# Performance work log

Hardware: AMD Instinct MI355X
Metric: run time of the kernel (lower is better)

The kernel has to match this reference:

```python
import jax, jax.numpy as jnp
import numpy as np

N_NODES = 100000
N_EDGES = 300000
N_GRAPHS = 2048
F_ATOM = 40
D_IN = 128    # GINInputSize
D_HID = 256   # GINHiddenSize
D_OUT = 512   # FPSize
D_TASK = 1    # OutputSize


def _glorot(key, shape):
    fan_in, fan_out = shape[0], shape[1]
    lim = (6.0 / (fan_in + fan_out)) ** 0.5
    return jax.random.uniform(key, shape, jnp.float32, -lim, lim)


def setup_inputs() -> dict:
    key = jax.random.key(0)
    ks = jax.random.split(key, 16)
    inp = {
        'x': jax.random.normal(ks[0], (N_NODES, F_ATOM), jnp.float32),
        'edge_index': jax.random.randint(ks[1], (2, N_EDGES), 0, N_NODES, jnp.int64),
        'batch': jnp.sort(jax.random.randint(ks[2], (N_NODES,), 0, N_GRAPHS, jnp.int64)),
        # NodeFeatEmbed: MLP([F_ATOM, D_IN]) == single Linear (plain_last)
        'W_embed': _glorot(ks[3], (F_ATOM, D_IN)),
        'b_embed': jnp.zeros((D_IN,), jnp.float32),
        # GINConv eps per layer (train_eps=False -> 0.0 constants)
        'eps': jnp.zeros((3,), jnp.float32),
        # layer 0: MLP([D_IN, D_HID, D_HID])
        'W1_0': _glorot(ks[4], (D_IN, D_HID)),  'b1_0': jnp.zeros((D_HID,), jnp.float32),
        'W2_0': _glorot(ks[5], (D_HID, D_HID)), 'b2_0': jnp.zeros((D_HID,), jnp.float32),
        # layer 1: MLP([D_HID, D_HID, D_HID])
        'W1_1': _glorot(ks[6], (D_HID, D_HID)), 'b1_1': jnp.zeros((D_HID,), jnp.float32),
        'W2_1': _glorot(ks[7], (D_HID, D_HID)), 'b2_1': jnp.zeros((D_HID,), jnp.float32),
        # layer 2 (last, maps to out_channels=FPSize): MLP([D_HID, D_OUT, D_OUT])
        'W1_2': _glorot(ks[8], (D_HID, D_OUT)), 'b1_2': jnp.zeros((D_OUT,), jnp.float32),
        'W2_2': _glorot(ks[9], (D_OUT, D_OUT)), 'b2_2': jnp.zeros((D_OUT,), jnp.float32),
        # task head
        'W_task': _glorot(ks[10], (D_OUT, D_TASK)),
        'b_task': jnp.zeros((D_TASK,), jnp.float32),
    }
    return inp


def _gin_forward(x, edge_index, batch, W_embed, b_embed, eps, layers, W_task, b_task):
    src, dst = edge_index[0], edge_index[1]
    # NodeFeatEmbed
    h = x @ W_embed + b_embed                                    # [N, D_IN]
    n_layers = len(layers)
    for l, (W1, b1, W2, b2) in enumerate(layers):
        # GINConv: MLP((1+eps)*h + sum_{j->i} h_j)
        agg = jax.ops.segment_sum(h[src], dst, num_segments=N_NODES)
        z = (1.0 + eps[l]) * h + agg
        h = jax.nn.relu(z @ W1 + b1) @ W2 + b2
        if l < n_layers - 1:                                     # inter-layer act (not after last)
            h = jax.nn.relu(h)
    # global_add_pool readout
    pooled = jax.ops.segment_sum(h, batch, num_segments=N_GRAPHS)  # [G, D_OUT]
    return pooled @ W_task + b_task                               # [G, D_TASK]


def reference(x, edge_index, batch, W_embed, b_embed, eps,
              W1_0, b1_0, W2_0, b2_0,
              W1_1, b1_1, W2_1, b2_1,
              W1_2, b1_2, W2_2, b2_2,
              W_task, b_task):
    layers = [(W1_0, b1_0, W2_0, b2_0), (W1_1, b1_1, W2_1, b2_1), (W1_2, b1_2, W2_2, b2_2)]
    return _gin_forward(x, edge_index, batch, W_embed, b_embed, eps, layers, W_task, b_task)
```

## Files before the change

kernel.cpp:

```cpp
#include <hip/hip_runtime.h>

#define N_NODES 100000
#define E_EDGES 300000
#define N_GRAPHS 2048

typedef float  floatx4 __attribute__((ext_vector_type(4)));
typedef short  shortx8 __attribute__((ext_vector_type(8)));

__device__ __forceinline__ float bf2f(unsigned short u) {
  return __uint_as_float(((unsigned int)u) << 16);
}
__device__ __forceinline__ unsigned short f2bf(float f) {
  unsigned int u = __float_as_uint(f);
  u += 0x7FFFu + ((u >> 16) & 1u);
  return (unsigned short)(u >> 16);
}

__device__ __forceinline__ void cp16(const void* g, void* l) {
  __builtin_amdgcn_global_load_lds(
      (const __attribute__((address_space(1))) unsigned int*)g,
      (__attribute__((address_space(3))) unsigned int*)l, 16, 0, 0);
}

struct PrepArgs {
  const float* W[4];
  unsigned short* Wt[4];
  int K[4];
  int N[4];
  const float* We;
  const float* be;
  const float* W1_0;
  unsigned short* WfT;
  const float* W2_2;
  const float* b2_2;
  const float* wtask;
  float* w2v;
  float* c2;
  float* nodedot;
  float* out;
  const float* b_task;
};

__global__ __launch_bounds__(256)
void prep_kernel(PrepArgs a) {
  const int blk = blockIdx.x;
  if (blk < 320) {
    int z, b;
    if (blk < 64)       { z = 0; b = blk; }
    else if (blk < 128) { z = 1; b = blk - 64; }
    else if (blk < 192) { z = 2; b = blk - 128; }
    else                { z = 3; b = blk - 192; }
    const int K = a.K[z], N = a.N[z];
    const int nt = N / 32;
    const int kb = (b / nt) * 32, nb = (b % nt) * 32;
    __shared__ unsigned short tile[32][33];
    const float* W = a.W[z];
    unsigned short* Wt = a.Wt[z];
    const int tx = threadIdx.x & 31, ty = threadIdx.x >> 5;
    for (int r = ty; r < 32; r += 8)
      tile[r][tx] = f2bf(W[(size_t)(kb + r) * N + nb + tx]);
    __syncthreads();
    for (int r = ty; r < 32; r += 8)
      Wt[(size_t)(nb + r) * K + kb + tx] = tile[tx][r];
  } else if (blk < 361) {
    const int k = blk - 320;
    const int n = threadIdx.x;
    if (k < 40) {
      float s = 0.f;
      for (int j = 0; j < 128; j++) s = fmaf(a.We[k * 128 + j], a.W1_0[(size_t)j * 256 + n], s);
      a.WfT[n * 64 + k] = f2bf(s);
    } else {
      float s = 0.f;
      for (int j = 0; j < 128; j++) s = fmaf(a.be[j], a.W1_0[(size_t)j * 256 + n], s);
      a.WfT[n * 64 + 40] = f2bf(s);
      for (int kk = 41; kk < 64; kk++) a.WfT[n * 64 + kk] = 0;
    }
  } else if (blk < 490) {
    const int p = blk - 361;
    const int lane = threadIdx.x & 63;
    const int wave = threadIdx.x >> 6;
    if (p < 128) {
      const int k = p * 4 + wave;
      const float* row = a.W2_2 + (size_t)k * 512 + lane * 8;
      float4 a0 = *(const float4*)(row);
      float4 a1 = *(const float4*)(row + 4);
      float4 w0 = *(const float4*)(a.wtask + lane * 8);
      float4 w1 = *(const float4*)(a.wtask + lane * 8 + 4);
      float s = a0.x * w0.x + a0.y * w0.y + a0.z * w0.z + a0.w * w0.w +
                a1.x * w1.x + a1.y * w1.y + a1.z * w1.z + a1.w * w1.w;
#pragma unroll
      for (int off = 32; off > 0; off >>= 1) s += __shfl_down(s, off);
      if (lane == 0) a.w2v[k] = s;
    } else if (wave == 0) {
      float4 a0 = *(const float4*)(a.b2_2 + lane * 8);
      float4 a1 = *(const float4*)(a.b2_2 + lane * 8 + 4);
      float4 w0 = *(const float4*)(a.wtask + lane * 8);
      float4 w1 = *(const float4*)(a.wtask + lane * 8 + 4);
      float s = a0.x * w0.x + a0.y * w0.y + a0.z * w0.z + a0.w * w0.w +
                a1.x * w1.x + a1.y * w1.y + a1.z * w1.z + a1.w * w1.w;
#pragma unroll
      for (int off = 32; off > 0; off >>= 1) s += __shfl_down(s, off);
      if (lane == 0) *a.c2 = s;
    }
  } else if (blk < 881) {
    int i = (blk - 490) * 256 + threadIdx.x;
    if (i < N_NODES) a.nodedot[i] = 0.f;
  } else {
    int g = (blk - 881) * 256 + threadIdx.x;
    if (g < N_GRAPHS) a.out[g] = a.b_task[0];
  }
}

__global__ __launch_bounds__(256)
void zero_kernel(int* __restrict__ p, int n) {
  int i = blockIdx.x * 256 + threadIdx.x;
  if (i < n) p[i] = 0;
}

__global__ __launch_bounds__(256)
void hist_kernel(const int* __restrict__ ei, int* __restrict__ deg) {
  int e = blockIdx.x * 256 + threadIdx.x;
  if (e < E_EDGES) atomicAdd(&deg[ei[E_EDGES + e]], 1);
}

__global__ __launch_bounds__(256)
void scan_blk_kernel(const int* __restrict__ in, int* __restrict__ out,
                     int* __restrict__ blk_sums, int n_in, int n_out) {
  __shared__ int sm[256];
  const int t = threadIdx.x;
  const int base = blockIdx.x * 1024 + t * 4;
  int d0 = (base + 0 < n_in) ? in[base + 0] : 0;
  int d1 = (base + 1 < n_in) ? in[base + 1] : 0;
  int d2 = (base + 2 < n_in) ? in[base + 2] : 0;
  int d3 = (base + 3 < n_in) ? in[base + 3] : 0;
  int s = d0 + d1 + d2 + d3;
  sm[t] = s;
  __syncthreads();
  for (int off = 1; off < 256; off <<= 1) {
    int v = (t >= off) ? sm[t - off] : 0;
    __syncthreads();
    sm[t] += v;
    __syncthreads();
  }
  int excl = sm[t] - s;
  if (base + 0 < n_out) out[base + 0] = excl;
  if (base + 1 < n_out) out[base + 1] = excl + d0;
  if (base + 2 < n_out) out[base + 2] = excl + d0 + d1;
  if (base + 3 < n_out) out[base + 3] = excl + d0 + d1 + d2;
  if (t == 255 && blk_sums) blk_sums[blockIdx.x] = sm[255];
}

__global__ __launch_bounds__(256)
void scan_fix_kernel(int* __restrict__ row_ptr, const int* __restrict__ blk_off,
                     int* __restrict__ cursor) {
  int i = blockIdx.x * 256 + threadIdx.x;
  if (i <= N_NODES) {
    int v = row_ptr[i] + blk_off[i >> 10];
    row_ptr[i] = v;
    if (i < N_NODES) cursor[i] = v;
  }
}

__global__ __launch_bounds__(256)
void fill_kernel(const int* __restrict__ ei, int* __restrict__ cursor,
                 int* __restrict__ csr_src) {
  int e = blockIdx.x * 256 + threadIdx.x;
  if (e < E_EDGES) {
    int d = ei[E_EDGES + e];
    int slot = atomicAdd(&cursor[d], 1);
    csr_src[slot] = ei[e];
  }
}

__global__ __launch_bounds__(256)
void gatherx_kernel(const float* __restrict__ X, unsigned short* __restrict__ G,
                    const int* __restrict__ row_ptr, const int* __restrict__ csr,
                    const float* __restrict__ eps) {
  const int node = blockIdx.x * 4 + (threadIdx.x >> 6);
  const int lane = threadIdx.x & 63;
  const float sc = 1.0f + eps[0];
  const int e0 = row_ptr[node];
  const int e1 = row_ptr[node + 1];
  float acc = 0.f;
  if (lane < 40) {
    acc = sc * X[(size_t)node * 40 + lane];
    int e = e0;
    for (; e + 4 <= e1; e += 4) {
      int s0 = csr[e], s1 = csr[e + 1], s2 = csr[e + 2], s3 = csr[e + 3];
      float a0 = X[(size_t)s0 * 40 + lane];
      float a1 = X[(size_t)s1 * 40 + lane];
      float a2 = X[(size_t)s2 * 40 + lane];
      float a3 = X[(size_t)s3 * 40 + lane];
      acc += (a0 + a1) + (a2 + a3);
    }
    for (; e < e1; e++)
      acc += X[(size_t)csr[e] * 40 + lane];
  } else if (lane == 40) {
    acc = sc + (float)(e1 - e0);
  }
  G[(size_t)node * 64 + lane] = f2bf(acc);
}

__global__ __launch_bounds__(256)
void gather_kernel(const unsigned short* __restrict__ H, unsigned short* __restrict__ Z,
                   const int* __restrict__ row_ptr, const int* __restrict__ csr,
                   const float* __restrict__ eps, int l) {
  const int node = blockIdx.x * 4 + (threadIdx.x >> 6);
  const int lane = threadIdx.x & 63;
  const float sc = 1.0f + eps[l];
  uint2 hv = *(const uint2*)(H + (size_t)node * 256 + lane * 4);
  float acc[4];
  acc[0] = sc * bf2f((unsigned short)(hv.x & 0xFFFF));
  acc[1] = sc * bf2f((unsigned short)(hv.x >> 16));
  acc[2] = sc * bf2f((unsigned short)(hv.y & 0xFFFF));
  acc[3] = sc * bf2f((unsigned short)(hv.y >> 16));
  const int e0 = row_ptr[node];
  const int e1 = row_ptr[node + 1];
  int e = e0;
  for (; e + 2 <= e1; e += 2) {
    int s0 = csr[e], s1 = csr[e + 1];
    uint2 a = *(const uint2*)(H + (size_t)s0 * 256 + lane * 4);
    uint2 b = *(const uint2*)(H + (size_t)s1 * 256 + lane * 4);
    acc[0] += bf2f((unsigned short)(a.x & 0xFFFF)) + bf2f((unsigned short)(b.x & 0xFFFF));
    acc[1] += bf2f((unsigned short)(a.x >> 16))    + bf2f((unsigned short)(b.x >> 16));
    acc[2] += bf2f((unsigned short)(a.y & 0xFFFF)) + bf2f((unsigned short)(b.y & 0xFFFF));
    acc[3] += bf2f((unsigned short)(a.y >> 16))    + bf2f((unsigned short)(b.y >> 16));
  }
  if (e < e1) {
    int s0 = csr[e];
    uint2 a = *(const uint2*)(H + (size_t)s0 * 256 + lane * 4);
    acc[0] += bf2f((unsigned short)(a.x & 0xFFFF));
    acc[1] += bf2f((unsigned short)(a.x >> 16));
    acc[2] += bf2f((unsigned short)(a.y & 0xFFFF));
    acc[3] += bf2f((unsigned short)(a.y >> 16));
  }
  unsigned short z[4] = {f2bf(acc[0]), f2bf(acc[1]), f2bf(acc[2]), f2bf(acc[3])};
  *(uint2*)(Z + (size_t)node * 256 + lane * 4) = *(uint2*)z;
}

template <int K1>
__global__ __launch_bounds__(256, 3)
void fused_mlp_kernel(const unsigned short* __restrict__ A,
                      const unsigned short* __restrict__ W1t,
                      const float* __restrict__ b1,
                      const unsigned short* __restrict__ W2t,
                      const float* __restrict__ b2,
                      unsigned short* __restrict__ H,
                      int M) {
  constexpr int ACH = K1 / 8;
  constexpr int ZP = (64 * ACH) / 256;

  __shared__ uint4 smem4[3072];
  unsigned short* Bs = (unsigned short*)smem4;
  unsigned short* Ts = (unsigned short*)(smem4 + 1024);

  const int m0 = blockIdx.x * 64;
  const int tid = threadIdx.x;
  const int lane = tid & 63;
  const int wave = tid >> 6;
  const int fr = lane & 15;
  const int fq = lane >> 4;
  const int wn = wave * 64;

#pragma unroll
  for (int p = 0; p < ZP; p++) {
    int slot = p * 256 + tid;
    int row = slot / ACH;
    int cs = slot % ACH;
    int cg = cs ^ (row & 7);
    int grow = m0 + row;
    if (grow >= M) grow = M - 1;
    cp16(A + (size_t)grow * K1 + cg * 8, Ts + (size_t)(p * 256 + wn) * 8);
  }

  const int bn_ = tid >> 2;
  const int bc_ = tid & 3;
  const unsigned short* srcW1[4];
  const unsigned short* srcW2[4];
#pragma unroll
  for (int p = 0; p < 4; p++) {
    int n = p * 64 + bn_;
    int sw = (bc_ ^ ((n >> 1) & 3)) << 3;
    srcW1[p] = W1t + (size_t)n * K1 + sw;
    srcW2[p] = W2t + (size_t)n * 256 + sw;
  }

  int offB[4];
#pragma unroll
  for (int j = 0; j < 4; j++) {
    int n = wn + j * 16 + fr;
    offB[j] = n * 32 + ((fq ^ ((n >> 1) & 3)) << 3);
  }

  floatx4 acc[4][4];
#pragma unroll
  for (int i = 0; i < 4; i++)
#pragma unroll
    for (int j = 0; j < 4; j++) acc[i][j] = (floatx4){0.f, 0.f, 0.f, 0.f};

  for (int k0 = 0; k0 < K1; k0 += 32) {
#pragma unroll
    for (int p = 0; p < 4; p++)
      cp16(srcW1[p] + k0, Bs + (size_t)(p * 256 + wn) * 8);
    __syncthreads();
    shortx8 af[4], bv[4];
    const int kc = k0 >> 3;
#pragma unroll
    for (int i = 0; i < 4; i++) {
      int row = i * 16 + fr;
      af[i] = *(const shortx8*)&Ts[row * K1 + (((kc + fq) ^ (fr & 7)) << 3)];
    }
#pragma unroll
    for (int j = 0; j < 4; j++) bv[j] = *(const shortx8*)&Bs[offB[j]];
#pragma unroll
    for (int i = 0; i < 4; i++)
#pragma unroll
      for (int j = 0; j < 4; j++)
        acc[i][j] = __builtin_amdgcn_mfma_f32_16x16x32_bf16(af[i], bv[j], acc[i][j], 0, 0, 0);
    __syncthreads();
  }

#pragma unroll
  for (int j = 0; j < 4; j++) {
    int col = wn + j * 16 + fr;
    float bb = b1[col];
    int cgc = col >> 3, c7 = col & 7;
#pragma unroll
    for (int i = 0; i < 4; i++)
#pragma unroll
      for (int r = 0; r < 4; r++) {
        int row = i * 16 + fq * 4 + r;
        float v = fmaxf(acc[i][j][r] + bb, 0.f);
        Ts[row * 256 + (((cgc ^ (row & 7)) << 3) | c7)] = f2bf(v);
        acc[i][j][r] = 0.f;
      }
  }

  for (int k0 = 0; k0 < 256; k0 += 32) {
#pragma unroll
    for (int p = 0; p < 4; p++)
      cp16(srcW2[p] + k0, Bs + (size_t)(p * 256 + wn) * 8);
    __syncthreads();
    shortx8 af[4], bv[4];
    const int kc = k0 >> 3;
#pragma unroll
    for (int i = 0; i < 4; i++) {
      int row = i * 16 + fr;
      af[i] = *(const shortx8*)&Ts[row * 256 + (((kc + fq) ^ (fr & 7)) << 3)];
    }
#pragma unroll
    for (int j = 0; j < 4; j++) bv[j] = *(const shortx8*)&Bs[offB[j]];
#pragma unroll
    for (int i = 0; i < 4; i++)
#pragma unroll
      for (int j = 0; j < 4; j++)
        acc[i][j] = __builtin_amdgcn_mfma_f32_16x16x32_bf16(af[i], bv[j], acc[i][j], 0, 0, 0);
    __syncthreads();
  }

#pragma unroll
  for (int j = 0; j < 4; j++) {
    int col = wn + j * 16 + fr;
    float bb = b2[col];
    int cgc = col >> 3, c7 = col & 7;
#pragma unroll
    for (int i = 0; i < 4; i++)
#pragma unroll
      for (int r = 0; r < 4; r++) {
        int row = i * 16 + fq * 4 + r;
        float v = fmaxf(acc[i][j][r] + bb, 0.f);
        Ts[row * 256 + (((cgc ^ (row & 7)) << 3) | c7)] = f2bf(v);
      }
  }
  __syncthreads();
  const int r2 = tid >> 5;
  const int cg2 = tid & 31;
#pragma unroll
  for (int p = 0; p < 8; p++) {
    int row = p * 8 + r2;
    int grow = m0 + row;
    if (grow < M) {
      uint4 v = *(const uint4*)&Ts[row * 256 + ((cg2 ^ (row & 7)) << 3)];
      *(uint4*)&H[(size_t)grow * 256 + cg2 * 8] = v;
    }
  }
}

__global__ __launch_bounds__(256, 3)
void fused_dot_kernel(const unsigned short* __restrict__ A,
                      const unsigned short* __restrict__ W1t,
                      const float* __restrict__ b1,
                      const float* __restrict__ w2v,
                      float* __restrict__ nodedot, int M) {
  __shared__ uint4 smem4[3072];
  unsigned short* Bs = (unsigned short*)smem4;
  unsigned short* Ts = (unsigned short*)(smem4 + 1024);

  const int m0 = blockIdx.x * 64;
  const int tid = threadIdx.x;
  const int lane = tid & 63;
  const int wave = tid >> 6;
  const int fr = lane & 15;
  const int fq = lane >> 4;
  const int wn = wave * 64;

#pragma unroll
  for (int p = 0; p < 8; p++) {
    int slot = p * 256 + tid;
    int row = slot >> 5;
    int cs = slot & 31;
    int cg = cs ^ (row & 7);
    int grow = m0 + row;
    if (grow >= M) grow = M - 1;
    cp16(A + (size_t)grow * 256 + cg * 8, Ts + (size_t)(p * 256 + wn) * 8);
  }

  const int bn_ = tid >> 2;
  const int bc_ = tid & 3;
  const unsigned short* srcW[4];
#pragma unroll
  for (int p = 0; p < 4; p++) {
    int n = p * 64 + bn_;
    srcW[p] = W1t + (size_t)n * 256 + ((bc_ ^ ((n >> 1) & 3)) << 3);
  }
  int offB[4];
#pragma unroll
  for (int j = 0; j < 4; j++) {
    int n = wn + j * 16 + fr;
    offB[j] = n * 32 + ((fq ^ ((n >> 1) & 3)) << 3);
  }

  float pd[4][4];
#pragma unroll
  for (int i = 0; i < 4; i++)
#pragma unroll
    for (int r = 0; r < 4; r++) pd[i][r] = 0.f;

  for (int nh = 0; nh < 2; nh++) {
    floatx4 acc[4][4];
#pragma unroll
    for (int i = 0; i < 4; i++)
#pragma unroll
      for (int j = 0; j < 4; j++) acc[i][j] = (floatx4){0.f, 0.f, 0.f, 0.f};
    const size_t nhoff = (size_t)nh * 256 * 256;
    for (int k0 = 0; k0 < 256; k0 += 32) {
#pragma unroll
      for (int p = 0; p < 4; p++)
        cp16(srcW[p] + nhoff + k0, Bs + (size_t)(p * 256 + wn) * 8);
      __syncthreads();
      shortx8 af[4], bv[4];
      const int kc = k0 >> 3;
#pragma unroll
      for (int i = 0; i < 4; i++) {
        int row = i * 16 + fr;
        af[i] = *(const shortx8*)&Ts[row * 256 + (((kc + fq) ^ (fr & 7)) << 3)];
      }
#pragma unroll
      for (int j = 0; j < 4; j++) bv[j] = *(const shortx8*)&Bs[offB[j]];
#pragma unroll
      for (int i = 0; i < 4; i++)
#pragma unroll
        for (int j = 0; j < 4; j++)
          acc[i][j] = __builtin_amdgcn_mfma_f32_16x16x32_bf16(af[i], bv[j], acc[i][j], 0, 0, 0);
      __syncthreads();
    }
#pragma unroll
    for (int j = 0; j < 4; j++) {
      int col = nh * 256 + wn + j * 16 + fr;
      float bb = b1[col];
      float wv = w2v[col];
#pragma unroll
      for (int i = 0; i < 4; i++)
#pragma unroll
        for (int r = 0; r < 4; r++)
          pd[i][r] += fmaxf(acc[i][j][r] + bb, 0.f) * wv;
    }
  }

#pragma unroll
  for (int i = 0; i < 4; i++)
#pragma unroll
    for (int r = 0; r < 4; r++) {
      float s = pd[i][r];
#pragma unroll
      for (int off = 1; off < 16; off <<= 1) s += __shfl_xor(s, off);
      if (fr == 0) {
        int row = m0 + i * 16 + fq * 4 + r;
        if (row < M) unsafeAtomicAdd(&nodedot[row], s);
      }
    }
}

__global__ __launch_bounds__(256)
void pool_kernel(const float* __restrict__ nodedot, const int* __restrict__ batch,
                 float* __restrict__ out, const float* __restrict__ c2p) {
  int t = blockIdx.x * 256 + threadIdx.x;
  int i0 = t * 64;
  if (i0 >= N_NODES) return;
  int i1 = i0 + 64;
  if (i1 > N_NODES) i1 = N_NODES;
  const float c2 = *c2p;
  int g = batch[i0];
  float s = 0.f;
  for (int i = i0; i < i1; i++) {
    int gi = batch[i];
    if (gi != g) { unsafeAtomicAdd(&out[g], s); g = gi; s = 0.f; }
    s += nodedot[i] + c2;
  }
  unsafeAtomicAdd(&out[g], s);
}

extern "C" void kernel_launch(void* const* d_in, const int* in_sizes, int n_in,
                              void* d_out, int out_size, void* d_ws, size_t ws_size,
                              hipStream_t stream) {
  const float* x       = (const float*)d_in[0];
  const int*   ei      = (const int*)d_in[1];
  const int*   batch   = (const int*)d_in[2];
  const float* W_embed = (const float*)d_in[3];
  const float* b_embed = (const float*)d_in[4];
  const float* eps     = (const float*)d_in[5];
  const float* W1[3] = {(const float*)d_in[6],  (const float*)d_in[10], (const float*)d_in[14]};
  const float* B1[3] = {(const float*)d_in[7],  (const float*)d_in[11], (const float*)d_in[15]};
  const float* W2[3] = {(const float*)d_in[8],  (const float*)d_in[12], (const float*)d_in[16]};
  const float* B2[3] = {(const float*)d_in[9],  (const float*)d_in[13], (const float*)d_in[17]};
  const float* W_task = (const float*)d_in[18];
  const float* b_task = (const float*)d_in[19];
  float* out = (float*)d_out;

  const size_t OFF_RZ  = 102400000;
  const size_t OFF_AUX = 153600000;
  if (ws_size < OFF_AUX + 4000000) return;
  unsigned short* RH = (unsigned short*)d_ws;
  unsigned short* RZ = (unsigned short*)((char*)d_ws + OFF_RZ);
  char* aux = (char*)d_ws + OFF_AUX;
  int* row_ptr  = (int*)(aux);
  int* cursor   = (int*)(aux + 400016);
  int* csr_src  = (int*)(aux + 800016);
  int* blk_sums = (int*)(aux + 2000016);
  int* blk_off  = (int*)(aux + 2000416);
  float* nodedot = (float*)(aux + 2000816);
  unsigned short* WT = (unsigned short*)(aux + 2400832);
  float* w2v = (float*)(aux + 3200832);
  float* c2  = (float*)(aux + 3202880);
  unsigned short* WfT    = WT;
  unsigned short* Wt2_0  = WT + 32768;
  unsigned short* Wt1_1  = WT + 98304;
  unsigned short* Wt2_1  = WT + 163840;
  unsigned short* Wt1_2  = WT + 229376;

  PrepArgs pa;
  pa.W[0] = W2[0]; pa.Wt[0] = Wt2_0; pa.K[0] = 256; pa.N[0] = 256;
  pa.W[1] = W1[1]; pa.Wt[1] = Wt1_1; pa.K[1] = 256; pa.N[1] = 256;
  pa.W[2] = W2[1]; pa.Wt[2] = Wt2_1; pa.K[2] = 256; pa.N[2] = 256;
  pa.W[3] = W1[2]; pa.Wt[3] = Wt1_2; pa.K[3] = 256; pa.N[3] = 512;
  pa.We = W_embed; pa.be = b_embed; pa.W1_0 = W1[0]; pa.WfT = WfT;
  pa.W2_2 = W2[2]; pa.b2_2 = B2[2]; pa.wtask = W_task; pa.w2v = w2v; pa.c2 = c2;
  pa.nodedot = nodedot; pa.out = out; pa.b_task = b_task;
  prep_kernel<<<889, 256, 0, stream>>>(pa);

  zero_kernel<<<(N_NODES + 255) / 256, 256, 0, stream>>>(cursor, N_NODES);
  hist_kernel<<<(E_EDGES + 255) / 256, 256, 0, stream>>>(ei, cursor);
  scan_blk_kernel<<<98, 256, 0, stream>>>(cursor, row_ptr, blk_sums, N_NODES, N_NODES + 1);
  scan_blk_kernel<<<1, 256, 0, stream>>>(blk_sums, blk_off, nullptr, 98, 98);
  scan_fix_kernel<<<(N_NODES + 256) / 256, 256, 0, stream>>>(row_ptr, blk_off, cursor);
  fill_kernel<<<(E_EDGES + 255) / 256, 256, 0, stream>>>(ei, cursor, csr_src);

  const int FB = (N_NODES + 63) / 64;

  gatherx_kernel<<<N_NODES / 4, 256, 0, stream>>>(x, RZ, row_ptr, csr_src, eps);
  fused_mlp_kernel<64><<<FB, 256, 0, stream>>>(RZ, WfT, B1[0], Wt2_0, B2[0], RH, N_NODES);

  gather_kernel<<<N_NODES / 4, 256, 0, stream>>>(RH, RZ, row_ptr, csr_src, eps, 1);
  fused_mlp_kernel<256><<<FB, 256, 0, stream>>>(RZ, Wt1_1, B1[1], Wt2_1, B2[1], RH, N_NODES);

  gather_kernel<<<N_NODES / 4, 256, 0, stream>>>(RH, RZ, row_ptr, csr_src, eps, 2);
  fused_dot_kernel<<<FB, 256, 0, stream>>>(RZ, Wt1_2, B1[2], w2v, nodedot, N_NODES);

  pool_kernel<<<((N_NODES + 63) / 64 + 255) / 256, 256, 0, stream>>>(nodedot, batch, out, c2);
}
```

Baseline: 422.0 us.

## Load weight fragments directly from global memory instead of staging through LDS

Both fused MLP kernels now read the B-operand (weight) fragments for the MFMA straight from global memory into registers, instead of copying each 32-wide K slice into a shared buffer. This drops the per-iteration barriers, shrinks LDS use from 48 KB to 32 KB, and fully unrolls the K loops. The aim is to remove the synchronisation and LDS traffic in the inner loop and allow more blocks per CU. The cost is that each wave issues its own global loads for weights, relying on L1/L2 hits, and load latency is exposed inside the unrolled loop.

```diff
diff --git a/kernel.cpp b/kernel.cpp
--- a/kernel.cpp
+++ b/kernel.cpp
@@ -250,9 +250,7 @@
   constexpr int ACH = K1 / 8;
   constexpr int ZP = (64 * ACH) / 256;
 
-  __shared__ uint4 smem4[3072];
-  unsigned short* Bs = (unsigned short*)smem4;
-  unsigned short* Ts = (unsigned short*)(smem4 + 1024);
+  __shared__ unsigned short Ts[64 * 256];
 
   const int m0 = blockIdx.x * 64;
   const int tid = threadIdx.x;
@@ -273,23 +271,13 @@
     cp16(A + (size_t)grow * K1 + cg * 8, Ts + (size_t)(p * 256 + wn) * 8);
   }
 
-  const int bn_ = tid >> 2;
-  const int bc_ = tid & 3;
-  const unsigned short* srcW1[4];
-  const unsigned short* srcW2[4];
-#pragma unroll
-  for (int p = 0; p < 4; p++) {
-    int n = p * 64 + bn_;
-    int sw = (bc_ ^ ((n >> 1) & 3)) << 3;
-    srcW1[p] = W1t + (size_t)n * K1 + sw;
-    srcW2[p] = W2t + (size_t)n * 256 + sw;
-  }
-
-  int offB[4];
+  const unsigned short* wb1[4];
+  const unsigned short* wb2[4];
 #pragma unroll
   for (int j = 0; j < 4; j++) {
     int n = wn + j * 16 + fr;
-    offB[j] = n * 32 + ((fq ^ ((n >> 1) & 3)) << 3);
+    wb1[j] = W1t + (size_t)n * K1 + fq * 8;
+    wb2[j] = W2t + (size_t)n * 256 + fq * 8;
   }
 
   floatx4 acc[4][4];
@@ -298,27 +286,26 @@
 #pragma unroll
     for (int j = 0; j < 4; j++) acc[i][j] = (floatx4){0.f, 0.f, 0.f, 0.f};
 
+  __syncthreads();
+
+#pragma unroll
   for (int k0 = 0; k0 < K1; k0 += 32) {
-#pragma unroll
-    for (int p = 0; p < 4; p++)
-      cp16(srcW1[p] + k0, Bs + (size_t)(p * 256 + wn) * 8);
-    __syncthreads();
     shortx8 af[4], bv[4];
     const int kc = k0 >> 3;
+#pragma unroll
+    for (int j = 0; j < 4; j++) bv[j] = *(const shortx8*)(wb1[j] + k0);
 #pragma unroll
     for (int i = 0; i < 4; i++) {
       int row = i * 16 + fr;
       af[i] = *(const shortx8*)&Ts[row * K1 + (((kc + fq) ^ (fr & 7)) << 3)];
     }
 #pragma unroll
-    for (int j = 0; j < 4; j++) bv[j] = *(const shortx8*)&Bs[offB[j]];
-#pragma unroll
     for (int i = 0; i < 4; i++)
 #pragma unroll
       for (int j = 0; j < 4; j++)
         acc[i][j] = __builtin_amdgcn_mfma_f32_16x16x32_bf16(af[i], bv[j], acc[i][j], 0, 0, 0);
-    __syncthreads();
-  }
+  }
+  __syncthreads();
 
 #pragma unroll
   for (int j = 0; j < 4; j++) {
@@ -335,28 +322,26 @@
         acc[i][j][r] = 0.f;
       }
   }
-
+  __syncthreads();
+
+#pragma unroll
   for (int k0 = 0; k0 < 256; k0 += 32) {
-#pragma unroll
-    for (int p = 0; p < 4; p++)
-      cp16(srcW2[p] + k0, Bs + (size_t)(p * 256 + wn) * 8);
-    __syncthreads();
     shortx8 af[4], bv[4];
     const int kc = k0 >> 3;
+#pragma unroll
+    for (int j = 0; j < 4; j++) bv[j] = *(const shortx8*)(wb2[j] + k0);
 #pragma unroll
     for (int i = 0; i < 4; i++) {
       int row = i * 16 + fr;
       af[i] = *(const shortx8*)&Ts[row * 256 + (((kc + fq) ^ (fr & 7)) << 3)];
     }
 #pragma unroll
-    for (int j = 0; j < 4; j++) bv[j] = *(const shortx8*)&Bs[offB[j]];
-#pragma unroll
     for (int i = 0; i < 4; i++)
 #pragma unroll
       for (int j = 0; j < 4; j++)
         acc[i][j] = __builtin_amdgcn_mfma_f32_16x16x32_bf16(af[i], bv[j], acc[i][j], 0, 0, 0);
-    __syncthreads();
-  }
+  }
+  __syncthreads();
 
 #pragma unroll
   for (int j = 0; j < 4; j++) {
@@ -392,9 +377,7 @@
                       const float* __restrict__ b1,
                       const float* __restrict__ w2v,
                       float* __restrict__ nodedot, int M) {
-  __shared__ uint4 smem4[3072];
-  unsigned short* Bs = (unsigned short*)smem4;
-  unsigned short* Ts = (unsigned short*)(smem4 + 1024);
+  __shared__ unsigned short Ts[64 * 256];
 
   const int m0 = blockIdx.x * 64;
   const int tid = threadIdx.x;
@@ -415,54 +398,42 @@
     cp16(A + (size_t)grow * 256 + cg * 8, Ts + (size_t)(p * 256 + wn) * 8);
   }
 
-  const int bn_ = tid >> 2;
-  const int bc_ = tid & 3;
-  const unsigned short* srcW[4];
-#pragma unroll
-  for (int p = 0; p < 4; p++) {
-    int n = p * 64 + bn_;
-    srcW[p] = W1t + (size_t)n * 256 + ((bc_ ^ ((n >> 1) & 3)) << 3);
-  }
-  int offB[4];
-#pragma unroll
-  for (int j = 0; j < 4; j++) {
-    int n = wn + j * 16 + fr;
-    offB[j] = n * 32 + ((fq ^ ((n >> 1) & 3)) << 3);
-  }
-
   float pd[4][4];
 #pragma unroll
   for (int i = 0; i < 4; i++)
 #pragma unroll
     for (int r = 0; r < 4; r++) pd[i][r] = 0.f;
 
+  __syncthreads();
+
   for (int nh = 0; nh < 2; nh++) {
+    const unsigned short* wb[4];
+#pragma unroll
+    for (int j = 0; j < 4; j++) {
+      int n = nh * 256 + wn + j * 16 + fr;
+      wb[j] = W1t + (size_t)n * 256 + fq * 8;
+    }
     floatx4 acc[4][4];
 #pragma unroll
     for (int i = 0; i < 4; i++)
 #pragma unroll
       for (int j = 0; j < 4; j++) acc[i][j] = (floatx4){0.f, 0.f, 0.f, 0.f};
-    const size_t nhoff = (size_t)nh * 256 * 256;
+#pragma unroll
     for (int k0 = 0; k0 < 256; k0 += 32) {
-#pragma unroll
-      for (int p = 0; p < 4; p++)
-        cp16(srcW[p] + nhoff + k0, Bs + (size_t)(p * 256 + wn) * 8);
-      __syncthreads();
       shortx8 af[4], bv[4];
       const int kc = k0 >> 3;
+#pragma unroll
+      for (int j = 0; j < 4; j++) bv[j] = *(const shortx8*)(wb[j] + k0);
 #pragma unroll
       for (int i = 0; i < 4; i++) {
         int row = i * 16 + fr;
         af[i] = *(const shortx8*)&Ts[row * 256 + (((kc + fq) ^ (fr & 7)) << 3)];
       }
 #pragma unroll
-      for (int j = 0; j < 4; j++) bv[j] = *(const shortx8*)&Bs[offB[j]];
-#pragma unroll
       for (int i = 0; i < 4; i++)
 #pragma unroll
         for (int j = 0; j < 4; j++)
           acc[i][j] = __builtin_amdgcn_mfma_f32_16x16x32_bf16(af[i], bv[j], acc[i][j], 0, 0, 0);
-      __syncthreads();
     }
 #pragma unroll
     for (int j = 0; j < 4; j++) {
```

Result: slower. 520.5 us (+23.3%).

## Double-buffer weight tiles in fused MLP kernels and drop node-dot atomics

Applied to the files above, without the earlier changes.

Weight k-tiles in LDS are now double-buffered in the fused MLP and fused dot kernels, so the next tile's async global-to-LDS copy overlaps the current MFMA step. The W2 prefetch is chained onto the end of the W1 loop. Each wave of the dot kernel writes its partial node dot to a separate slab instead of atomically adding into one array, and the pool kernel sums the four slabs. The larger LDS footprint forces launch bounds down to 2 blocks per CU, trading occupancy for overlap.

```diff
diff --git a/kernel.cpp b/kernel.cpp
--- a/kernel.cpp
+++ b/kernel.cpp
@@ -239,7 +239,7 @@
 }
 
 template <int K1>
-__global__ __launch_bounds__(256, 3)
+__global__ __launch_bounds__(256, 2)
 void fused_mlp_kernel(const unsigned short* __restrict__ A,
                       const unsigned short* __restrict__ W1t,
                       const float* __restrict__ b1,
@@ -249,10 +249,10 @@
                       int M) {
   constexpr int ACH = K1 / 8;
   constexpr int ZP = (64 * ACH) / 256;
-
-  __shared__ uint4 smem4[3072];
-  unsigned short* Bs = (unsigned short*)smem4;
-  unsigned short* Ts = (unsigned short*)(smem4 + 1024);
+  constexpr int NT1 = K1 / 32;
+
+  __shared__ unsigned short Bs[2][256 * 32];
+  __shared__ unsigned short Ts[64 * 256];
 
   const int m0 = blockIdx.x * 64;
   const int tid = threadIdx.x;
@@ -292,32 +292,45 @@
     offB[j] = n * 32 + ((fq ^ ((n >> 1) & 3)) << 3);
   }
 
+#pragma unroll
+  for (int p = 0; p < 4; p++)
+    cp16(srcW1[p], &Bs[0][(size_t)(p * 256 + wn) * 8]);
+
   floatx4 acc[4][4];
 #pragma unroll
   for (int i = 0; i < 4; i++)
 #pragma unroll
     for (int j = 0; j < 4; j++) acc[i][j] = (floatx4){0.f, 0.f, 0.f, 0.f};
 
-  for (int k0 = 0; k0 < K1; k0 += 32) {
-#pragma unroll
-    for (int p = 0; p < 4; p++)
-      cp16(srcW1[p] + k0, Bs + (size_t)(p * 256 + wn) * 8);
-    __syncthreads();
+  __syncthreads();
+  int buf = 0;
+
+  for (int t = 0; t < NT1; t++) {
+    if (t + 1 < NT1) {
+#pragma unroll
+      for (int p = 0; p < 4; p++)
+        cp16(srcW1[p] + (t + 1) * 32, &Bs[buf ^ 1][(size_t)(p * 256 + wn) * 8]);
+    } else {
+#pragma unroll
+      for (int p = 0; p < 4; p++)
+        cp16(srcW2[p], &Bs[buf ^ 1][(size_t)(p * 256 + wn) * 8]);
+    }
     shortx8 af[4], bv[4];
-    const int kc = k0 >> 3;
+    const int kc = t * 4;
 #pragma unroll
     for (int i = 0; i < 4; i++) {
       int row = i * 16 + fr;
       af[i] = *(const shortx8*)&Ts[row * K1 + (((kc + fq) ^ (fr & 7)) << 3)];
     }
 #pragma unroll
-    for (int j = 0; j < 4; j++) bv[j] = *(const shortx8*)&Bs[offB[j]];
+    for (int j = 0; j < 4; j++) bv[j] = *(const shortx8*)&Bs[buf][offB[j]];
 #pragma unroll
     for (int i = 0; i < 4; i++)
 #pragma unroll
       for (int j = 0; j < 4; j++)
         acc[i][j] = __builtin_amdgcn_mfma_f32_16x16x32_bf16(af[i], bv[j], acc[i][j], 0, 0, 0);
     __syncthreads();
+    buf ^= 1;
   }
 
 #pragma unroll
@@ -335,27 +348,30 @@
         acc[i][j][r] = 0.f;
       }
   }
-
-  for (int k0 = 0; k0 < 256; k0 += 32) {
-#pragma unroll
-    for (int p = 0; p < 4; p++)
-      cp16(srcW2[p] + k0, Bs + (size_t)(p * 256 + wn) * 8);
-    __syncthreads();
+  __syncthreads();
+
+  for (int t = 0; t < 8; t++) {
+    if (t + 1 < 8) {
+#pragma unroll
+      for (int p = 0; p < 4; p++)
+        cp16(srcW2[p] + (t + 1) * 32, &Bs[buf ^ 1][(size_t)(p * 256 + wn) * 8]);
+    }
     shortx8 af[4], bv[4];
-    const int kc = k0 >> 3;
+    const int kc = t * 4;
 #pragma unroll
     for (int i = 0; i < 4; i++) {
       int row = i * 16 + fr;
       af[i] = *(const shortx8*)&Ts[row * 256 + (((kc + fq) ^ (fr & 7)) << 3)];
     }
 #pragma unroll
-    for (int j = 0; j < 4; j++) bv[j] = *(const shortx8*)&Bs[offB[j]];
+    for (int j = 0; j < 4; j++) bv[j] = *(const shortx8*)&Bs[buf][offB[j]];
 #pragma unroll
     for (int i = 0; i < 4; i++)
 #pragma unroll
       for (int j = 0; j < 4; j++)
         acc[i][j] = __builtin_amdgcn_mfma_f32_16x16x32_bf16(af[i], bv[j], acc[i][j], 0, 0, 0);
     __syncthreads();
+    buf ^= 1;
   }
 
 #pragma unroll
@@ -386,15 +402,14 @@
   }
 }
 
-__global__ __launch_bounds__(256, 3)
+__global__ __launch_bounds__(256, 2)
 void fused_dot_kernel(const unsigned short* __restrict__ A,
                       const unsigned short* __restrict__ W1t,
                       const float* __restrict__ b1,
                       const float* __restrict__ w2v,
-                      float* __restrict__ nodedot, int M) {
-  __shared__ uint4 smem4[3072];
-  unsigned short* Bs = (unsigned short*)smem4;
-  unsigned short* Ts = (unsigned short*)(smem4 + 1024);
+                      float* __restrict__ nodedot4, int M) {
+  __shared__ unsigned short Bs[2][256 * 32];
+  __shared__ unsigned short Ts[64 * 256];
 
   const int m0 = blockIdx.x * 64;
   const int tid = threadIdx.x;
@@ -430,50 +445,65 @@
     offB[j] = n * 32 + ((fq ^ ((n >> 1) & 3)) << 3);
   }
 
+#pragma unroll
+  for (int p = 0; p < 4; p++)
+    cp16(srcW[p], &Bs[0][(size_t)(p * 256 + wn) * 8]);
+
   float pd[4][4];
 #pragma unroll
   for (int i = 0; i < 4; i++)
 #pragma unroll
     for (int r = 0; r < 4; r++) pd[i][r] = 0.f;
 
-  for (int nh = 0; nh < 2; nh++) {
-    floatx4 acc[4][4];
+  floatx4 acc[4][4];
+#pragma unroll
+  for (int i = 0; i < 4; i++)
+#pragma unroll
+    for (int j = 0; j < 4; j++) acc[i][j] = (floatx4){0.f, 0.f, 0.f, 0.f};
+
+  __syncthreads();
+  int buf = 0;
+
+  for (int s = 0; s < 16; s++) {
+    int ns = s + 1;
+    if (ns < 16) {
+      const size_t off = (size_t)(ns >> 3) * 65536 + (size_t)(ns & 7) * 32;
+#pragma unroll
+      for (int p = 0; p < 4; p++)
+        cp16(srcW[p] + off, &Bs[buf ^ 1][(size_t)(p * 256 + wn) * 8]);
+    }
+    shortx8 af[4], bv[4];
+    const int kc = (s & 7) * 4;
+#pragma unroll
+    for (int i = 0; i < 4; i++) {
+      int row = i * 16 + fr;
+      af[i] = *(const shortx8*)&Ts[row * 256 + (((kc + fq) ^ (fr & 7)) << 3)];
+    }
+#pragma unroll
+    for (int j = 0; j < 4; j++) bv[j] = *(const shortx8*)&Bs[buf][offB[j]];
 #pragma unroll
     for (int i = 0; i < 4; i++)
 #pragma unroll
-      for (int j = 0; j < 4; j++) acc[i][j] = (floatx4){0.f, 0.f, 0.f, 0.f};
-    const size_t nhoff = (size_t)nh * 256 * 256;
-    for (int k0 = 0; k0 < 256; k0 += 32) {
-#pragma unroll
-      for (int p = 0; p < 4; p++)
-        cp16(srcW[p] + nhoff + k0, Bs + (size_t)(p * 256 + wn) * 8);
-      __syncthreads();
-      shortx8 af[4], bv[4];
-      const int kc = k0 >> 3;
-#pragma unroll
-      for (int i = 0; i < 4; i++) {
-        int row = i * 16 + fr;
-        af[i] = *(const shortx8*)&Ts[row * 256 + (((kc + fq) ^ (fr & 7)) << 3)];
+      for (int j = 0; j < 4; j++)
+        acc[i][j] = __builtin_amdgcn_mfma_f32_16x16x32_bf16(af[i], bv[j], acc[i][j], 0, 0, 0);
+    __syncthreads();
+    buf ^= 1;
+
+    if ((s & 7) == 7) {
+      const int nh = s >> 3;
+#pragma unroll
+      for (int j = 0; j < 4; j++) {
+        int col = nh * 256 + wn + j * 16 + fr;
+        float bb = b1[col];
+        float wv = w2v[col];
+#pragma unroll
+        for (int i = 0; i < 4; i++)
+#pragma unroll
+          for (int r = 0; r < 4; r++) {
+            pd[i][r] += fmaxf(acc[i][j][r] + bb, 0.f) * wv;
+            acc[i][j][r] = 0.f;
+          }
       }
-#pragma unroll
-      for (int j = 0; j < 4; j++) bv[j] = *(const shortx8*)&Bs[offB[j]];
-#pragma unroll
-      for (int i = 0; i < 4; i++)
-#pragma unroll
-        for (int j = 0; j < 4; j++)
-          acc[i][j] = __builtin_amdgcn_mfma_f32_16x16x32_bf16(af[i], bv[j], acc[i][j], 0, 0, 0);
-      __syncthreads();
-    }
-#pragma unroll
-    for (int j = 0; j < 4; j++) {
-      int col = nh * 256 + wn + j * 16 + fr;
-      float bb = b1[col];
-      float wv = w2v[col];
-#pragma unroll
-      for (int i = 0; i < 4; i++)
-#pragma unroll
-        for (int r = 0; r < 4; r++)
-          pd[i][r] += fmaxf(acc[i][j][r] + bb, 0.f) * wv;
     }
   }
 
@@ -486,13 +516,13 @@
       for (int off = 1; off < 16; off <<= 1) s += __shfl_xor(s, off);
       if (fr == 0) {
         int row = m0 + i * 16 + fq * 4 + r;
-        if (row < M) unsafeAtomicAdd(&nodedot[row], s);
+        if (row < M) nodedot4[(size_t)wave * N_NODES + row] = s;
       }
     }
 }
 
 __global__ __launch_bounds__(256)
-void pool_kernel(const float* __restrict__ nodedot, const int* __restrict__ batch,
+void pool_kernel(const float* __restrict__ nodedot4, const int* __restrict__ batch,
                  float* __restrict__ out, const float* __restrict__ c2p) {
   int t = blockIdx.x * 256 + threadIdx.x;
   int i0 = t * 64;
@@ -505,7 +535,9 @@
   for (int i = i0; i < i1; i++) {
     int gi = batch[i];
     if (gi != g) { unsafeAtomicAdd(&out[g], s); g = gi; s = 0.f; }
-    s += nodedot[i] + c2;
+    float nd = (nodedot4[i] + nodedot4[N_NODES + i]) +
+               (nodedot4[2 * N_NODES + i] + nodedot4[3 * N_NODES + i]);
+    s += nd + c2;
   }
   unsafeAtomicAdd(&out[g], s);
 }
@@ -527,10 +559,12 @@
   const float* b_task = (const float*)d_in[19];
   float* out = (float*)d_out;
 
+  const size_t OFF_ND4 = 51200000;
   const size_t OFF_RZ  = 102400000;
   const size_t OFF_AUX = 153600000;
   if (ws_size < OFF_AUX + 4000000) return;
   unsigned short* RH = (unsigned short*)d_ws;
+  float* nodedot4 = (float*)((char*)d_ws + OFF_ND4);
   unsigned short* RZ = (unsigned short*)((char*)d_ws + OFF_RZ);
   char* aux = (char*)d_ws + OFF_AUX;
   int* row_ptr  = (int*)(aux);
@@ -574,7 +608,7 @@
   fused_mlp_kernel<256><<<FB, 256, 0, stream>>>(RZ, Wt1_1, B1[1], Wt2_1, B2[1], RH, N_NODES);
 
   gather_kernel<<<N_NODES / 4, 256, 0, stream>>>(RH, RZ, row_ptr, csr_src, eps, 2);
-  fused_dot_kernel<<<FB, 256, 0, stream>>>(RZ, Wt1_2, B1[2], w2v, nodedot, N_NODES);
-
-  pool_kernel<<<((N_NODES + 63) / 64 + 255) / 256, 256, 0, stream>>>(nodedot, batch, out, c2);
-}
+  fused_dot_kernel<<<FB, 256, 0, stream>>>(RZ, Wt1_2, B1[2], w2v, nodedot4, N_NODES);
+
+  pool_kernel<<<((N_NODES + 63) / 64 + 255) / 256, 256, 0, stream>>>(nodedot4, batch, out, c2);
+}
```

New measurement: 464.9 us. 1.1x slower.
